# Performance work log

Measured on AMD Instinct MI355X. Metric: run time of the kernel, lower is better.

Reference implementation:

```python
import jax, jax.numpy as jnp
import numpy as np

NUM_HEADS = 16
D_MODEL = 1024
D_K = D_MODEL // NUM_HEADS


def setup_inputs() -> dict:
    key = jax.random.key(0)
    ks = jax.random.split(key, 11)
    B, S, D = 4, 2048, D_MODEL
    s = 1.0 / np.sqrt(D)
    return {
        "query": jax.random.normal(ks[0], (B, S, D), jnp.float32),
        "key": jax.random.normal(ks[1], (B, S, D), jnp.float32),
        "value": jax.random.normal(ks[2], (B, S, D), jnp.float32),
        "Wq": jax.random.normal(ks[3], (D, D), jnp.float32) * s,
        "bq": jnp.zeros((D,), jnp.float32),
        "Wk": jax.random.normal(ks[4], (D, D), jnp.float32) * s,
        "bk": jnp.zeros((D,), jnp.float32),
        "Wv": jax.random.normal(ks[5], (D, D), jnp.float32) * s,
        "bv": jnp.zeros((D,), jnp.float32),
        "Wo": jax.random.normal(ks[6], (D, D), jnp.float32) * s,
        "bo": jnp.zeros((D,), jnp.float32),
    }


def reference(query, key, value, Wq, bq, Wk, bk, Wv, bv, Wo, bo):
    B, S, D = query.shape
    H, dk = NUM_HEADS, D_K
    # linear projections (torch Linear: x @ W.T + b)
    q = query @ Wq.T + bq
    k = key @ Wk.T + bk
    v = value @ Wv.T + bv
    # [B, S, D] -> [B, H, S, dk]
    q = q.reshape(B, S, H, dk).transpose(0, 2, 1, 3)
    k = k.reshape(B, S, H, dk).transpose(0, 2, 1, 3)
    v = v.reshape(B, S, H, dk).transpose(0, 2, 1, 3)
    # scaled dot-product attention (explicit scores, no mask, dropout unused in fwd)
    scores = jnp.einsum("bhqd,bhkd->bhqk", q, k) / jnp.sqrt(jnp.float32(dk))
    attn = jax.nn.softmax(scores, axis=-1)
    out = jnp.einsum("bhqk,bhkd->bhqd", attn, v)
    out = out.transpose(0, 2, 1, 3).reshape(B, S, D)
    return out @ Wo.T + bo
```

## Files before the change

kernel.cpp:

```cpp
#include <hip/hip_runtime.h>
#include <cstdint>
#include <cstddef>

typedef __bf16 bf16_t;
typedef __bf16 bf16x8 __attribute__((ext_vector_type(8)));
typedef __bf16 bf16x4 __attribute__((ext_vector_type(4)));
typedef float f32x4 __attribute__((ext_vector_type(4)));

static constexpr int SEQ = 2048;
static constexpr int DMODEL = 1024;
static constexpr int HEADS = 16;
static constexpr int DK = 64;
static constexpr int MROWS = 4 * SEQ;
static constexpr size_t NEC = (size_t)MROWS * DMODEL;
static constexpr size_t WEC = (size_t)DMODEL * DMODEL;

__global__ __launch_bounds__(256) void cast_all(const float* __restrict__ q,
                                                const float* __restrict__ k,
                                                const float* __restrict__ v,
                                                const float* __restrict__ wq,
                                                const float* __restrict__ wk,
                                                const float* __restrict__ wv,
                                                const float* __restrict__ wo,
                                                bf16_t* __restrict__ out) {
  size_t i = (size_t)blockIdx.x * 256 + threadIdx.x;
  size_t e = i * 8;
  const float* src;
  size_t off;
  if (e < NEC) { src = q; off = e; }
  else if (e < 2 * NEC) { src = k; off = e - NEC; }
  else if (e < 3 * NEC) { src = v; off = e - 2 * NEC; }
  else if (e < 3 * NEC + WEC) { src = wq; off = e - 3 * NEC; }
  else if (e < 3 * NEC + 2 * WEC) { src = wk; off = e - 3 * NEC - WEC; }
  else if (e < 3 * NEC + 3 * WEC) { src = wv; off = e - 3 * NEC - 2 * WEC; }
  else { src = wo; off = e - 3 * NEC - 3 * WEC; }
  const float4* p = reinterpret_cast<const float4*>(src + off);
  float4 a = p[0], b = p[1];
  bf16x8 o;
  o[0] = (bf16_t)a.x; o[1] = (bf16_t)a.y; o[2] = (bf16_t)a.z; o[3] = (bf16_t)a.w;
  o[4] = (bf16_t)b.x; o[5] = (bf16_t)b.y; o[6] = (bf16_t)b.z; o[7] = (bf16_t)b.w;
  *(reinterpret_cast<bf16x8*>(out + e)) = o;
}

__device__ __forceinline__ void async16(const bf16_t* g, bf16_t* l) {
  __builtin_amdgcn_global_load_lds((const __attribute__((address_space(1))) void*)g,
                                   (__attribute__((address_space(3))) void*)l,
                                   16, 0, 0);
}

__device__ __forceinline__ int lds_off(int m, int l4) {
  int lr = m >> 1;
  return lr * 64 + (((((m & 1) << 2) | l4) ^ (lr & 7)) << 3);
}

__global__ __launch_bounds__(512, 4) void gemm_qkv(const bf16_t* __restrict__ Abase,
                                                   const bf16_t* __restrict__ Wbase,
                                                   const float* __restrict__ bq,
                                                   const float* __restrict__ bk,
                                                   const float* __restrict__ bv,
                                                   float scaleQ,
                                                   bf16_t* __restrict__ QKbase,
                                                   bf16_t* __restrict__ Vt) {
  __shared__ __align__(16) bf16_t smem[24576];
  bf16_t* sAb = smem;
  bf16_t* sBb = smem + 8192;
  const int tid = threadIdx.x;
  const int lane = tid & 63;
  const int w = tid >> 6;
  const int wm = w >> 2, wn = w & 3;
  const int l16 = lane & 15, l4 = lane >> 4;

  int bid = blockIdx.x;
  int swz = (bid & 7) * 96 + (bid >> 3);
  const int seg = swz >> 8;
  const int inner = swz & 255;
  const bf16_t* A = Abase + (size_t)seg * NEC;
  const bf16_t* Bw = Wbase + (size_t)seg * WEC;
  const float* bias = seg == 0 ? bq : (seg == 1 ? bk : bv);
  const float scale = seg == 0 ? scaleQ : 1.0f;
  const int bm = inner >> 2, bn = inner & 3;
  const int m0 = bm << 7, n0 = bn << 8;

  const int sg = (lane & 7) ^ ((lane >> 3) & 7);
  const int mS = 2 * (w * 8 + (lane >> 3)) + (sg >> 2);
  const int gS = (sg & 3) * 8;

  f32x4 acc[4][4] = {};

  auto stage = [&](int bb, int k0) {
    async16(A + (size_t)(m0 + mS) * DMODEL + k0 + gS, &sAb[bb * 4096 + w * 512]);
    async16(Bw + (size_t)(n0 + mS) * DMODEL + k0 + gS, &sBb[bb * 8192 + w * 512]);
    async16(Bw + (size_t)(n0 + 128 + mS) * DMODEL + k0 + gS, &sBb[bb * 8192 + 4096 + w * 512]);
  };

  stage(0, 0);
  __syncthreads();
  const int NKT = DMODEL / 32;
  for (int t = 0; t < NKT; ++t) {
    if (t + 1 < NKT) stage((t + 1) & 1, (t + 1) * 32);
    const bf16_t* bA = &sAb[(t & 1) * 4096];
    const bf16_t* bB = &sBb[(t & 1) * 8192];
    bf16x8 af[4], bf[4];
#pragma unroll
    for (int f = 0; f < 4; ++f)
      af[f] = *reinterpret_cast<const bf16x8*>(&bA[lds_off(wm * 64 + f * 16 + l16, l4)]);
#pragma unroll
    for (int j = 0; j < 4; ++j)
      bf[j] = *reinterpret_cast<const bf16x8*>(&bB[lds_off(wn * 64 + j * 16 + l16, l4)]);
    __builtin_amdgcn_s_setprio(1);
#pragma unroll
    for (int i = 0; i < 4; ++i)
#pragma unroll
      for (int j = 0; j < 4; ++j)
        acc[i][j] = __builtin_amdgcn_mfma_f32_16x16x32_bf16(af[i], bf[j], acc[i][j], 0, 0, 0);
    __builtin_amdgcn_s_setprio(0);
    __syncthreads();
  }

  float bj[4];
#pragma unroll
  for (int j = 0; j < 4; ++j) bj[j] = bias[n0 + wn * 64 + j * 16 + l16];

  const int hglob = bn * 4 + wn;
  bf16_t* patch = smem + w * 3072;

  if (seg < 2) {
    bf16_t* outQK = QKbase + (size_t)seg * NEC;
#pragma unroll
    for (int h2 = 0; h2 < 2; ++h2) {
#pragma unroll
      for (int ii = 0; ii < 2; ++ii) {
        int i = h2 * 2 + ii;
#pragma unroll
        for (int j = 0; j < 4; ++j) {
#pragma unroll
          for (int r = 0; r < 4; ++r) {
            float v = (acc[i][j][r] + bj[j]) * scale;
            patch[(ii * 16 + l4 * 4 + r) * 72 + j * 16 + l16] = (bf16_t)v;
          }
        }
      }
#pragma unroll
      for (int kk = 0; kk < 4; ++kk) {
        int row = kk * 8 + (lane >> 3);
        int doff = (lane & 7) * 8;
        bf16x8 ch = *reinterpret_cast<const bf16x8*>(&patch[row * 72 + doff]);
        int m = m0 + wm * 64 + h2 * 32 + row;
        int b = m >> 11, s = m & 2047;
        *reinterpret_cast<bf16x8*>(
            &outQK[(((size_t)(b * HEADS + hglob) * SEQ + s) << 6) + doff]) = ch;
      }
    }
  } else {
#pragma unroll
    for (int h2 = 0; h2 < 2; ++h2) {
#pragma unroll
      for (int ii = 0; ii < 2; ++ii) {
        int i = h2 * 2 + ii;
#pragma unroll
        for (int j = 0; j < 4; ++j) {
          bf16x4 pk;
#pragma unroll
          for (int r = 0; r < 4; ++r) pk[r] = (bf16_t)(acc[i][j][r] + bj[j]);
          *reinterpret_cast<bf16x4*>(
              &patch[(j * 16 + l16) * 48 + ii * 16 + l4 * 4]) = pk;
        }
      }
#pragma unroll
      for (int kk = 0; kk < 4; ++kk) {
        int d = kk * 16 + (lane >> 2);
        int soff = (lane & 3) * 8;
        bf16x8 ch = *reinterpret_cast<const bf16x8*>(&patch[d * 48 + soff]);
        int m = m0 + wm * 64 + h2 * 32;
        int b = m >> 11, s = (m & 2047) + soff;
        *reinterpret_cast<bf16x8*>(
            &Vt[((size_t)(b * HEADS + hglob) * DK + d) * SEQ + s]) = ch;
      }
    }
  }
}

__global__ __launch_bounds__(256, 4) void gemm_out(const bf16_t* __restrict__ A,
                                                   const bf16_t* __restrict__ Bw,
                                                   const float* __restrict__ bias,
                                                   float* __restrict__ Cout) {
  __shared__ __align__(16) bf16_t sA[2][128 * 32];
  __shared__ __align__(16) bf16_t sB[2][128 * 32];
  const int tid = threadIdx.x;
  const int lane = tid & 63;
  const int wv = tid >> 6;
  const int l16 = lane & 15, l4 = lane >> 4;

  int bid = blockIdx.x;
  int swz = (bid & 7) * 64 + (bid >> 3);
  const int bm = swz >> 3, bn = swz & 7;
  const int m0 = bm << 7, n0 = bn << 7;
  const int wr = (wv >> 1) * 64, wc = (wv & 1) * 64;

  const int sg = (lane & 7) ^ ((lane >> 3) & 7);
  const int mS = 2 * (wv * 8 + (lane >> 3)) + (sg >> 2);
  const int gS = (sg & 3) * 8;

  f32x4 acc[4][4] = {};

  auto stage = [&](int bb, int k0) {
#pragma unroll
    for (int c = 0; c < 2; ++c) {
      async16(A + (size_t)(m0 + c * 64 + mS) * DMODEL + k0 + gS, &sA[bb][c * 2048 + wv * 512]);
      async16(Bw + (size_t)(n0 + c * 64 + mS) * DMODEL + k0 + gS, &sB[bb][c * 2048 + wv * 512]);
    }
  };

  stage(0, 0);
  __syncthreads();
  const int NKT = DMODEL / 32;
  for (int t = 0; t < NKT; ++t) {
    if (t + 1 < NKT) stage((t + 1) & 1, (t + 1) * 32);
    const bf16_t* bA = sA[t & 1];
    const bf16_t* bB = sB[t & 1];
    bf16x8 afrag[4], bfrag[4];
#pragma unroll
    for (int f = 0; f < 4; ++f) {
      afrag[f] = *reinterpret_cast<const bf16x8*>(&bA[lds_off(wr + f * 16 + l16, l4)]);
      bfrag[f] = *reinterpret_cast<const bf16x8*>(&bB[lds_off(wc + f * 16 + l16, l4)]);
    }
    __builtin_amdgcn_s_setprio(1);
#pragma unroll
    for (int i = 0; i < 4; ++i)
#pragma unroll
      for (int j = 0; j < 4; ++j)
        acc[i][j] = __builtin_amdgcn_mfma_f32_16x16x32_bf16(afrag[i], bfrag[j], acc[i][j], 0, 0, 0);
    __builtin_amdgcn_s_setprio(0);
    __syncthreads();
  }

  float bj[4];
#pragma unroll
  for (int j = 0; j < 4; ++j) bj[j] = bias[n0 + wc + j * 16 + l16];

#pragma unroll
  for (int i = 0; i < 4; ++i) {
#pragma unroll
    for (int j = 0; j < 4; ++j) {
#pragma unroll
      for (int r = 0; r < 4; ++r) {
        int m = m0 + wr + i * 16 + l4 * 4 + r;
        int n = n0 + wc + j * 16 + l16;
        Cout[(size_t)m * DMODEL + n] = acc[i][j][r] + bj[j];
      }
    }
  }
}

__device__ __forceinline__ int kvsrc_row(int r) {
  return (r & 32) | (((r >> 3) & 1) << 4) | (((r >> 2) & 1) << 3) |
         (((r >> 4) & 1) << 2) | (r & 3);
}

__global__ __launch_bounds__(512, 2) void attn_kernel(const bf16_t* __restrict__ Q,
                                                      const bf16_t* __restrict__ Kp,
                                                      const bf16_t* __restrict__ Vt,
                                                      bf16_t* __restrict__ AO) {
  __shared__ __align__(16) bf16_t sK[2][64 * 64];
  __shared__ __align__(16) bf16_t sV[2][64 * 64];
  const int tid = threadIdx.x;
  const int lane = tid & 63;
  const int wv = tid >> 6;
  const int l16 = lane & 15, l4 = lane >> 4;
  const int sub8 = lane >> 3, c8 = lane & 7;

  const int nq = SEQ / 256;
  int bid = blockIdx.x;
  int swz = (bid & 7) * 64 + (bid >> 3);
  const int bh = swz / nq, qt = swz % nq;
  const int b = bh >> 4, h = bh & 15;
  const bf16_t* Qh = Q + (size_t)bh * SEQ * DK;
  const bf16_t* Kh = Kp + (size_t)bh * SEQ * DK;
  const bf16_t* Vh = Vt + (size_t)bh * DK * SEQ;
  const int q0 = qt * 256 + wv * 32;

  bf16x8 aq[2][2];
#pragma unroll
  for (int s = 0; s < 2; ++s)
#pragma unroll
    for (int hf = 0; hf < 2; ++hf)
      aq[s][hf] = *reinterpret_cast<const bf16x8*>(
          &Qh[(size_t)(q0 + s * 16 + l16) * DK + hf * 32 + l4 * 8]);

  bf16x8 ones;
#pragma unroll
  for (int i = 0; i < 8; ++i) ones[i] = (bf16_t)1.0f;

  f32x4 o[2][4] = {};
  f32x4 lacc[2] = {};

  auto stage = [&](int buf, int kv0) {
    int r = wv * 8 + sub8;
    int kvr = kvsrc_row(r);
    int cs = (c8 ^ sub8) << 3;
    async16(Kh + (size_t)(kv0 + kvr) * DK + cs, &sK[buf][wv * 512]);
    async16(Vh + (size_t)r * SEQ + kv0 + cs, &sV[buf][wv * 512]);
  };

  auto compute = [&](int buf) {
    const bf16_t* bK = sK[buf];
    const bf16_t* bV = sV[buf];
    f32x4 sc[2][4] = {};
    __builtin_amdgcn_s_setprio(1);
#pragma unroll
    for (int t = 0; t < 4; ++t) {
      bf16x8 kf0 = *reinterpret_cast<const bf16x8*>(
          &bK[(t * 16 + l16) * 64 + ((l4 ^ (l16 & 7)) << 3)]);
      bf16x8 kf1 = *reinterpret_cast<const bf16x8*>(
          &bK[(t * 16 + l16) * 64 + (((4 + l4) ^ (l16 & 7)) << 3)]);
#pragma unroll
      for (int s = 0; s < 2; ++s) {
        sc[s][t] = __builtin_amdgcn_mfma_f32_16x16x32_bf16(kf0, aq[s][0], sc[s][t], 0, 0, 0);
        sc[s][t] = __builtin_amdgcn_mfma_f32_16x16x32_bf16(kf1, aq[s][1], sc[s][t], 0, 0, 0);
      }
    }
    __builtin_amdgcn_s_setprio(0);
    bf16x8 pa[2][2];
#pragma unroll
    for (int s = 0; s < 2; ++s) {
#pragma unroll
      for (int t = 0; t < 4; ++t) {
#pragma unroll
        for (int j = 0; j < 4; ++j) {
          pa[s][t >> 1][(t & 1) * 4 + j] = (bf16_t)__builtin_amdgcn_exp2f(sc[s][t][j]);
        }
      }
    }
    __builtin_amdgcn_s_setprio(1);
#pragma unroll
    for (int nb = 0; nb < 4; ++nb) {
      bf16x8 vf0 = *reinterpret_cast<const bf16x8*>(
          &bV[(nb * 16 + l16) * 64 + ((l4 ^ (l16 & 7)) << 3)]);
      bf16x8 vf1 = *reinterpret_cast<const bf16x8*>(
          &bV[(nb * 16 + l16) * 64 + (((4 + l4) ^ (l16 & 7)) << 3)]);
#pragma unroll
      for (int s = 0; s < 2; ++s) {
        o[s][nb] = __builtin_amdgcn_mfma_f32_16x16x32_bf16(pa[s][0], vf0, o[s][nb], 0, 0, 0);
        o[s][nb] = __builtin_amdgcn_mfma_f32_16x16x32_bf16(pa[s][1], vf1, o[s][nb], 0, 0, 0);
      }
    }
#pragma unroll
    for (int s = 0; s < 2; ++s) {
      lacc[s] = __builtin_amdgcn_mfma_f32_16x16x32_bf16(pa[s][0], ones, lacc[s], 0, 0, 0);
      lacc[s] = __builtin_amdgcn_mfma_f32_16x16x32_bf16(pa[s][1], ones, lacc[s], 0, 0, 0);
    }
    __builtin_amdgcn_s_setprio(0);
  };

  stage(0, 0);
  __syncthreads();
  const int NT = SEQ / 64;
  for (int it = 0; it < NT; ++it) {
    if (it + 1 < NT) stage((it + 1) & 1, (it + 1) * 64);
    compute(it & 1);
    __syncthreads();
  }

#pragma unroll
  for (int s = 0; s < 2; ++s) {
#pragma unroll
    for (int j = 0; j < 4; ++j) {
      float inv = 1.0f / lacc[s][j];
      int qrow = q0 + s * 16 + l4 * 4 + j;
#pragma unroll
      for (int nb = 0; nb < 4; ++nb)
        AO[((size_t)(b * SEQ + qrow)) * DMODEL + h * DK + nb * 16 + l16] =
            (bf16_t)(o[s][nb][j] * inv);
    }
  }
}

extern "C" void kernel_launch(void* const* d_in, const int* in_sizes, int n_in,
                              void* d_out, int out_size, void* d_ws, size_t ws_size,
                              hipStream_t stream) {
  const float* query = (const float*)d_in[0];
  const float* key_i = (const float*)d_in[1];
  const float* value = (const float*)d_in[2];
  const float* Wq = (const float*)d_in[3];
  const float* bq = (const float*)d_in[4];
  const float* Wk = (const float*)d_in[5];
  const float* bk = (const float*)d_in[6];
  const float* Wv = (const float*)d_in[7];
  const float* bv = (const float*)d_in[8];
  const float* Wo = (const float*)d_in[9];
  const float* bo = (const float*)d_in[10];
  float* out = (float*)d_out;

  bf16_t* qb = (bf16_t*)d_ws;
  bf16_t* wqb = qb + 3 * NEC;
  bf16_t* wob = wqb + 3 * WEC;
  bf16_t* Qp = wob + WEC;
  bf16_t* Kp = Qp + NEC;
  bf16_t* Vt = Kp + NEC;
  bf16_t* AO = Vt + NEC;

  size_t totE = 3 * NEC + 4 * WEC;
  cast_all<<<dim3((unsigned)(totE / 8 / 256)), dim3(256), 0, stream>>>(
      query, key_i, value, Wq, Wk, Wv, Wo, qb);

  const float cexp = 0.18033688f;
  gemm_qkv<<<dim3(768), dim3(512), 0, stream>>>(qb, wqb, bq, bk, bv, cexp, Qp, Vt);

  attn_kernel<<<dim3(4 * HEADS * (SEQ / 256)), 512, 0, stream>>>(Qp, Kp, Vt, AO);

  gemm_out<<<dim3(512), dim3(256), 0, stream>>>(AO, wob, bo, out);
}
```

Baseline: 179.8 us.

## Fuse fp32-to-bf16 activation cast into QKV GEMM A-tile loading

The separate cast of the query, key and value activations to bf16 is removed. The QKV GEMM now loads the fp32 activation tiles into registers, converts them, and writes them to LDS after the MFMA block, software-pipelined one k-step ahead. Only the weights are still cast in a standalone kernel. This drops a full read/write pass over the activations and the bf16 staging buffer. In exchange the A operand moves from async global-to-LDS loads to register-staged loads that need twice the global bandwidth per tile, which adds register pressure.

```diff
diff --git a/kernel.cpp b/kernel.cpp
--- a/kernel.cpp
+++ b/kernel.cpp
@@ -15,25 +15,19 @@
 static constexpr size_t NEC = (size_t)MROWS * DMODEL;
 static constexpr size_t WEC = (size_t)DMODEL * DMODEL;
 
-__global__ __launch_bounds__(256) void cast_all(const float* __restrict__ q,
-                                                const float* __restrict__ k,
-                                                const float* __restrict__ v,
-                                                const float* __restrict__ wq,
-                                                const float* __restrict__ wk,
-                                                const float* __restrict__ wv,
-                                                const float* __restrict__ wo,
-                                                bf16_t* __restrict__ out) {
+__global__ __launch_bounds__(256) void cast_w(const float* __restrict__ wq,
+                                              const float* __restrict__ wk,
+                                              const float* __restrict__ wv,
+                                              const float* __restrict__ wo,
+                                              bf16_t* __restrict__ out) {
   size_t i = (size_t)blockIdx.x * 256 + threadIdx.x;
   size_t e = i * 8;
   const float* src;
   size_t off;
-  if (e < NEC) { src = q; off = e; }
-  else if (e < 2 * NEC) { src = k; off = e - NEC; }
-  else if (e < 3 * NEC) { src = v; off = e - 2 * NEC; }
-  else if (e < 3 * NEC + WEC) { src = wq; off = e - 3 * NEC; }
-  else if (e < 3 * NEC + 2 * WEC) { src = wk; off = e - 3 * NEC - WEC; }
-  else if (e < 3 * NEC + 3 * WEC) { src = wv; off = e - 3 * NEC - 2 * WEC; }
-  else { src = wo; off = e - 3 * NEC - 3 * WEC; }
+  if (e < WEC) { src = wq; off = e; }
+  else if (e < 2 * WEC) { src = wk; off = e - WEC; }
+  else if (e < 3 * WEC) { src = wv; off = e - 2 * WEC; }
+  else { src = wo; off = e - 3 * WEC; }
   const float4* p = reinterpret_cast<const float4*>(src + off);
   float4 a = p[0], b = p[1];
   bf16x8 o;
@@ -53,7 +47,9 @@
   return lr * 64 + (((((m & 1) << 2) | l4) ^ (lr & 7)) << 3);
 }
 
-__global__ __launch_bounds__(512, 4) void gemm_qkv(const bf16_t* __restrict__ Abase,
+__global__ __launch_bounds__(512, 4) void gemm_qkv(const float* __restrict__ Aq,
+                                                   const float* __restrict__ Ak,
+                                                   const float* __restrict__ Av,
                                                    const bf16_t* __restrict__ Wbase,
                                                    const float* __restrict__ bq,
                                                    const float* __restrict__ bk,
@@ -74,7 +70,7 @@
   int swz = (bid & 7) * 96 + (bid >> 3);
   const int seg = swz >> 8;
   const int inner = swz & 255;
-  const bf16_t* A = Abase + (size_t)seg * NEC;
+  const float* Afp = seg == 0 ? Aq : (seg == 1 ? Ak : Av);
   const bf16_t* Bw = Wbase + (size_t)seg * WEC;
   const float* bias = seg == 0 ? bq : (seg == 1 ? bk : bv);
   const float scale = seg == 0 ? scaleQ : 1.0f;
@@ -86,18 +82,34 @@
   const int gS = (sg & 3) * 8;
 
   f32x4 acc[4][4] = {};
-
-  auto stage = [&](int bb, int k0) {
-    async16(A + (size_t)(m0 + mS) * DMODEL + k0 + gS, &sAb[bb * 4096 + w * 512]);
+  float4 ra0, ra1;
+
+  auto loadA = [&](int k0) {
+    const float* p = Afp + (size_t)(m0 + mS) * DMODEL + k0 + gS;
+    ra0 = *reinterpret_cast<const float4*>(p);
+    ra1 = *reinterpret_cast<const float4*>(p + 4);
+  };
+  auto writeA = [&](int bb) {
+    bf16x8 o;
+    o[0] = (bf16_t)ra0.x; o[1] = (bf16_t)ra0.y; o[2] = (bf16_t)ra0.z; o[3] = (bf16_t)ra0.w;
+    o[4] = (bf16_t)ra1.x; o[5] = (bf16_t)ra1.y; o[6] = (bf16_t)ra1.z; o[7] = (bf16_t)ra1.w;
+    *reinterpret_cast<bf16x8*>(&sAb[bb * 4096 + w * 512 + lane * 8]) = o;
+  };
+  auto stageB = [&](int bb, int k0) {
     async16(Bw + (size_t)(n0 + mS) * DMODEL + k0 + gS, &sBb[bb * 8192 + w * 512]);
     async16(Bw + (size_t)(n0 + 128 + mS) * DMODEL + k0 + gS, &sBb[bb * 8192 + 4096 + w * 512]);
   };
 
-  stage(0, 0);
+  loadA(0);
+  stageB(0, 0);
+  writeA(0);
   __syncthreads();
   const int NKT = DMODEL / 32;
   for (int t = 0; t < NKT; ++t) {
-    if (t + 1 < NKT) stage((t + 1) & 1, (t + 1) * 32);
+    if (t + 1 < NKT) {
+      loadA((t + 1) * 32);
+      stageB((t + 1) & 1, (t + 1) * 32);
+    }
     const bf16_t* bA = &sAb[(t & 1) * 4096];
     const bf16_t* bB = &sBb[(t & 1) * 8192];
     bf16x8 af[4], bf[4];
@@ -114,6 +126,7 @@
       for (int j = 0; j < 4; ++j)
         acc[i][j] = __builtin_amdgcn_mfma_f32_16x16x32_bf16(af[i], bf[j], acc[i][j], 0, 0, 0);
     __builtin_amdgcn_s_setprio(0);
+    if (t + 1 < NKT) writeA((t + 1) & 1);
     __syncthreads();
   }
 
@@ -391,20 +404,19 @@
   const float* bo = (const float*)d_in[10];
   float* out = (float*)d_out;
 
-  bf16_t* qb = (bf16_t*)d_ws;
-  bf16_t* wqb = qb + 3 * NEC;
+  bf16_t* wqb = (bf16_t*)d_ws;
   bf16_t* wob = wqb + 3 * WEC;
   bf16_t* Qp = wob + WEC;
   bf16_t* Kp = Qp + NEC;
   bf16_t* Vt = Kp + NEC;
   bf16_t* AO = Vt + NEC;
 
-  size_t totE = 3 * NEC + 4 * WEC;
-  cast_all<<<dim3((unsigned)(totE / 8 / 256)), dim3(256), 0, stream>>>(
-      query, key_i, value, Wq, Wk, Wv, Wo, qb);
+  cast_w<<<dim3((unsigned)(4 * WEC / 8 / 256)), dim3(256), 0, stream>>>(
+      Wq, Wk, Wv, Wo, wqb);
 
   const float cexp = 0.18033688f;
-  gemm_qkv<<<dim3(768), dim3(512), 0, stream>>>(qb, wqb, bq, bk, bv, cexp, Qp, Vt);
+  gemm_qkv<<<dim3(768), dim3(512), 0, stream>>>(query, key_i, value, wqb,
+                                                bq, bk, bv, cexp, Qp, Vt);
 
   attn_kernel<<<dim3(4 * HEADS * (SEQ / 256)), 512, 0, stream>>>(Qp, Kp, Vt, AO);
 
```

After: 168.3 us. 1.07x faster.
